# Kernel tuning notes

Measured on AMD Instinct MI355X. Metric: run time of the kernel, lower is better.

The kernel has to match this reference:

```python
import jax, jax.numpy as jnp
import numpy as np

NUM_HEADS = 8
NUM_LEVELS = 4
NUM_POINTS = 16
NUM_BEV = 2
EMBED = 256
BS = 64
NQ = NUM_LEVELS * NUM_POINTS  # 64


def _bilinear_sample(img, grid):
    """F.grid_sample(mode='bilinear', padding_mode='zeros', align_corners=False).
    img: (N, C, H, W); grid: (N, Hg, Wg, 2) in [-1, 1] (x, y). Returns (N, C, Hg, Wg)."""
    N, C, H, W = img.shape
    gx = (grid[..., 0] + 1.0) * (W * 0.5) - 0.5  # (N, Hg, Wg)
    gy = (grid[..., 1] + 1.0) * (H * 0.5) - 0.5
    x0 = jnp.floor(gx)
    y0 = jnp.floor(gy)
    flat = img.reshape(N, C, H * W)

    def gather(xi, yi):
        valid = (xi >= 0) & (xi <= W - 1) & (yi >= 0) & (yi <= H - 1)
        xc = jnp.clip(xi, 0, W - 1).astype(jnp.int32)
        yc = jnp.clip(yi, 0, H - 1).astype(jnp.int32)
        idx = (yc * W + xc).reshape(N, 1, -1)
        g = jnp.take_along_axis(flat, idx, axis=2).reshape(N, C, xi.shape[1], xi.shape[2])
        return g * valid[:, None, :, :].astype(img.dtype)

    wx1 = (gx - x0)[:, None]  # (N,1,Hg,Wg)
    wy1 = (gy - y0)[:, None]
    v00 = gather(x0, y0)
    v01 = gather(x0 + 1.0, y0)
    v10 = gather(x0, y0 + 1.0)
    v11 = gather(x0 + 1.0, y0 + 1.0)
    top = v00 * (1.0 - wx1) + v01 * wx1
    bot = v10 * (1.0 - wx1) + v11 * wx1
    return top * (1.0 - wy1) + bot * wy1


def _forward(query, key_hist, value_hist, reference_points, W_off, b_off, spatial_shapes):
    bs, nq, d = query.shape
    Hn, L, P, BEV = NUM_HEADS, NUM_LEVELS, NUM_POINTS, NUM_BEV
    dh = d // Hn
    Pb = P * BEV
    ss = np.asarray(spatial_shapes)  # (L, 2) static (h, w)

    queries = jnp.concatenate([query, query], axis=1)           # (bs, 2*nq, d)
    keies = jnp.concatenate([query, key_hist], axis=1)
    values = jnp.concatenate([query, value_hist], axis=1)
    qb = queries.shape[1]

    # sampling offsets projection (the only used learned linear in the original forward)
    off = (queries @ W_off + b_off).reshape(bs, qb, Hn, Pb, L, 2)

    # NOTE: original re-assigns q/k/v from the RAW concatenated tensors (to_Q/to_K/to_V discarded)
    qh = queries.reshape(bs, qb, Hn, dh)
    kh = keies.reshape(bs, qb, Hn, dh)
    vh = values.reshape(bs, qb, Hn, dh)

    attn = jax.nn.softmax(jnp.einsum('bqhd,bkhd->bqhk', qh, kh), axis=-1)
    attn = attn.reshape(bs, qb, Hn, L, Pb)

    rp = jnp.concatenate([reference_points, reference_points], axis=1)  # (bs, qb, L, 2)
    norm = jnp.stack([jnp.asarray(ss[:, 1], jnp.float32),
                      jnp.asarray(ss[:, 0], jnp.float32)], axis=-1)      # (L, 2) = (w, h)
    loc = rp[:, :, None, None, :, :] + off / norm                        # (bs,qb,H,Pb,L,2)
    # FAITHFUL: original uses .view here (pure reshape, not a transpose)
    loc = loc.reshape(bs, qb, Hn, L, Pb, 2)
    grids = 2.0 * loc - 1.0

    sampled = []
    start = 0
    for l in range(L):
        h_, w_ = int(ss[l, 0]), int(ss[l, 1])
        vl = vh[:, start:start + h_ * w_]                                # (bs, hw, H, dh)
        start += h_ * w_
        img = vl.transpose(0, 2, 3, 1).reshape(bs * Hn, dh, h_, w_)      # (bs*H, dh, h, w)
        grid_l = grids[:, :, :, l].transpose(0, 2, 1, 3, 4).reshape(bs * Hn, qb, Pb, 2)
        sampled.append(_bilinear_sample(img, grid_l))                    # (bs*H, dh, qb, Pb)

    samp = jnp.stack(sampled, axis=-2).reshape(bs * Hn, dh, qb, L * Pb)
    aw = attn.transpose(0, 2, 1, 3, 4).reshape(bs * Hn, 1, qb, L * Pb)
    out = (samp * aw).sum(-1)                                            # (bs*H, dh, qb)
    # FAITHFUL: original reshapes q_bev dim as (nq, BEV) and means over BEV
    out = out.reshape(bs, Hn * dh, nq, BEV).mean(-1).transpose(0, 2, 1)  # (bs, nq, d)
    return out + query  # dropout is identity at eval


def setup_inputs() -> dict:
    key = jax.random.key(0)
    ks = jax.random.split(key, 6)
    query = jax.random.normal(ks[0], (BS, NQ, EMBED), jnp.float32)
    key_hist = jax.random.normal(ks[1], (BS, NQ, EMBED), jnp.float32)
    value_hist = jax.random.normal(ks[2], (BS, NQ, EMBED), jnp.float32)
    reference_points = jax.random.uniform(ks[3], (BS, NQ, NUM_LEVELS, 2), jnp.float32)
    spatial_shapes = jnp.array([[4, 8]] * NUM_LEVELS, dtype=jnp.int32)  # sum(h*w)=128=L*P*BEV
    off_dim = NUM_HEADS * NUM_BEV * NUM_POINTS * NUM_LEVELS * 2
    W_off = jax.random.normal(ks[4], (EMBED, off_dim), jnp.float32) * 0.02
    b_off = jnp.zeros((off_dim,), jnp.float32)
    return {"query": query, "key_hist": key_hist, "value_hist": value_hist,
            "reference_points": reference_points, "spatial_shapes": spatial_shapes,
            "W_off": W_off, "b_off": b_off}


def reference(query, key_hist, value_hist, reference_points, spatial_shapes, W_off, b_off):
    return _forward(query, key_hist, value_hist, reference_points, W_off, b_off, spatial_shapes)
```

## Files before the change

### kernel.cpp

```cpp
#include <hip/hip_runtime.h>


typedef short  s16x8 __attribute__((ext_vector_type(8)));
typedef short  s16x4 __attribute__((ext_vector_type(4)));
typedef float  f32x4 __attribute__((ext_vector_type(4)));

__device__ __forceinline__ unsigned short f2bf(float f) {
    union { float f; unsigned u; } v; v.f = f;
    unsigned r = v.u + 0x7FFFu + ((v.u >> 16) & 1u);
    return (unsigned short)(r >> 16);
}
__device__ __forceinline__ float bf2f(unsigned short u) {
    return __uint_as_float(((unsigned)u) << 16);
}

__global__ __launch_bounds__(256) void prep(
    const float* __restrict__ W, const float* __restrict__ query,
    const float* __restrict__ key_hist,
    short* __restrict__ Wtb, short* __restrict__ Qb, short* __restrict__ Khb)
{
    __shared__ float s[32][33];
    const int bx = blockIdx.x, t = threadIdx.x;
    if (bx < 512) {
        const int n0 = (bx & 63) * 32, k0 = (bx >> 6) * 32;
        const int c = t & 31, r0 = t >> 5;
        #pragma unroll
        for (int p = 0; p < 4; ++p) {
            const int r = r0 + p * 8;
            s[r][c] = W[(size_t)(k0 + r) * 2048 + n0 + c];
        }
        __syncthreads();
        #pragma unroll
        for (int p = 0; p < 4; ++p) {
            const int r = r0 + p * 8;
            Wtb[(size_t)(n0 + r) * 256 + k0 + c] = (short)f2bf(s[c][r]);
        }
    } else {
        const int j = bx - 512;
        const bool isK = j >= 1024;
        const float* src = isK ? key_hist : query;
        short* dst = isK ? Khb : Qb;
        const int i4 = ((j & 1023) * 256 + t) * 4;
        const float4 v = *(const float4*)(src + i4);
        s16x4 o;
        o.x = (short)f2bf(v.x); o.y = (short)f2bf(v.y);
        o.z = (short)f2bf(v.z); o.w = (short)f2bf(v.w);
        *(s16x4*)(dst + i4) = o;
    }
}

__global__ __launch_bounds__(256, 2) void mega2(
    const float* __restrict__ query, const float* __restrict__ value_hist,
    const float* __restrict__ refp,
    const short* __restrict__ Qb, const short* __restrict__ Khb,
    const short* __restrict__ Wtb, const float* __restrict__ bias,
    float* __restrict__ out)
{
    const int h = blockIdx.x, b = blockIdx.y;
    const int t = threadIdx.x, lane = t & 63, wave = t >> 6;
    const int quad = lane >> 4, col = lane & 15;
    const int wq = wave * 16;

    __shared__ __align__(16) short VTl[32 * 136];
    __shared__ __align__(16) short attLb[64 * 136];
    __shared__ __align__(16) float rpsL[512];
    __shared__ __align__(16) float AmU[9216];
    short* Bsl = (short*)AmU;
    float* Am  = AmU;
    short* Amb = (short*)AmU;

    {
        const int p = t >> 1, hf = (t & 1) * 16;
        const float* src = ((p < 64) ? query : value_hist) +
                           (size_t)(b * 64 + (p & 63)) * 256 + h * 32 + hf;
        #pragma unroll
        for (int u = 0; u < 4; ++u) {
            const float4 v = *(const float4*)(src + 4 * u);
            VTl[(hf + 4 * u + 0) * 136 + p] = (short)f2bf(v.x);
            VTl[(hf + 4 * u + 1) * 136 + p] = (short)f2bf(v.y);
            VTl[(hf + 4 * u + 2) * 136 + p] = (short)f2bf(v.z);
            VTl[(hf + 4 * u + 3) * 136 + p] = (short)f2bf(v.w);
        }
    }
    rpsL[t]       = refp[(size_t)b * 512 + t];
    rpsL[t + 256] = refp[(size_t)b * 512 + t + 256];

    {
        const s16x8 aq = *(const s16x8*)(Qb +
            ((size_t)b * 64 + wq + col) * 256 + h * 32 + quad * 8);
        f32x4 lacc[8];
        #pragma unroll
        for (int t8 = 0; t8 < 8; ++t8) {
            const short* src = (t8 < 4)
                ? (Qb  + ((size_t)b * 64 + 16 * t8 + col) * 256)
                : (Khb + ((size_t)b * 64 + 16 * (t8 - 4) + col) * 256);
            const s16x8 bk = *(const s16x8*)(src + h * 32 + quad * 8);
            const f32x4 z = {0.f, 0.f, 0.f, 0.f};
            lacc[t8] = __builtin_amdgcn_mfma_f32_16x16x32_bf16(aq, bk, z, 0, 0, 0);
        }
        #pragma unroll
        for (int r = 0; r < 4; ++r) {
            float m = lacc[0][r];
            #pragma unroll
            for (int t8 = 1; t8 < 8; ++t8) m = fmaxf(m, lacc[t8][r]);
            #pragma unroll
            for (int s = 1; s < 16; s <<= 1) m = fmaxf(m, __shfl_xor(m, s, 64));
            float e[8], ssum = 0.f;
            #pragma unroll
            for (int t8 = 0; t8 < 8; ++t8) {
                e[t8] = __expf(lacc[t8][r] - m); ssum += e[t8];
            }
            #pragma unroll
            for (int s = 1; s < 16; s <<= 1) ssum += __shfl_xor(ssum, s, 64);
            const float inv = 1.0f / ssum;
            const int q = wq + 4 * quad + r;
            #pragma unroll
            for (int t8 = 0; t8 < 8; ++t8)
                attLb[q * 136 + 16 * t8 + col] = (short)f2bf(e[t8] * inv);
        }
    }

    f32x4 acc[4][4] = {};
    for (int kq = 0; kq < 4; ++kq) {
        s16x8 afp[4][2];
        #pragma unroll
        for (int mi = 0; mi < 4; ++mi)
            #pragma unroll
            for (int ks = 0; ks < 2; ++ks)
                afp[mi][ks] = *(const s16x8*)(Qb +
                    ((size_t)b * 64 + 16 * mi + col) * 256
                    + kq * 64 + ks * 32 + quad * 8);
        #pragma unroll
        for (int u = 0; u < 8; ++u) {
            const int g = t + 256 * u;
            const int w = g >> 9, rowu = (g >> 3) & 63, koff = (g & 7) * 8;
            *(s16x8*)&Bsl[(w * 64 + rowu) * 72 + koff] =
                *(const s16x8*)(Wtb + (size_t)(h * 256 + w * 64 + rowu) * 256
                                + kq * 64 + koff);
        }
        __syncthreads();
        #pragma unroll
        for (int ks = 0; ks < 2; ++ks) {
            s16x8 bf[4];
            #pragma unroll
            for (int nj = 0; nj < 4; ++nj)
                bf[nj] = *(const s16x8*)&Bsl[(wave * 64 + 16 * nj + col) * 72
                                             + ks * 32 + quad * 8];
            #pragma unroll
            for (int mi = 0; mi < 4; ++mi)
                #pragma unroll
                for (int nj = 0; nj < 4; ++nj)
                    acc[mi][nj] = __builtin_amdgcn_mfma_f32_16x16x32_bf16(
                        afp[mi][ks], bf[nj], acc[mi][nj], 0, 0, 0);
        }
        __syncthreads();
    }

    {
        #pragma unroll
        for (int u = 0; u < 33; ++u) AmU[t + 256 * u] = 0.f;
    }
    __syncthreads();
    {
        const int i   = col >> 1;
        const int par = col & 1;
        const int base = 32 * wave;
        #pragma unroll
        for (int nj = 0; nj < 4; ++nj) {
            const float bj = bias[h * 256 + wave * 64 + 16 * nj + col];
            const int f = 32 * wave + 8 * nj + i;
            #pragma unroll
            for (int mi = 0; mi < 4; ++mi) {
                float v[4], p[4];
                #pragma unroll
                for (int r = 0; r < 4; ++r) v[r] = acc[mi][nj][r] + bj;
                #pragma unroll
                for (int r = 0; r < 4; ++r) p[r] = __shfl_xor(v[r], 1, 64);
                #pragma unroll
                for (int rs = 0; rs < 2; ++rs) {
                    const int r = par * 2 + rs;
                    const float ox = par ? p[r] : v[r];
                    const float oy = par ? v[r] : p[r];
                    const int q = 16 * mi + 4 * quad + r;
                    const float2 rp = *(const float2*)&rpsL[q * 8 + (i & 3) * 2];
                    const float a = bf2f((unsigned short)attLb[q * 136 + f]);
                    const float gx = 8.f * (rp.x + ox * 0.125f) - 0.5f;
                    const float gy = 4.f * (rp.y + oy * 0.25f) - 0.5f;
                    const float x0f = floorf(gx), y0f = floorf(gy);
                    const float wx = gx - x0f, wy = gy - y0f;
                    const int x0 = (int)x0f, y0 = (int)y0f;
                    float* rowW = &Am[q * 132 + base];
                    const bool xv0 = (x0 >= 0) && (x0 < 8);
                    const bool xv1 = (x0 >= -1) && (x0 < 7);
                    const bool yv0 = (y0 >= 0) && (y0 < 4);
                    const bool yv1 = (y0 >= -1) && (y0 < 3);
                    if (xv0 && yv0) unsafeAtomicAdd(&rowW[y0 * 8 + x0],           a * (1.f - wx) * (1.f - wy));
                    if (xv1 && yv0) unsafeAtomicAdd(&rowW[y0 * 8 + x0 + 1],       a * wx * (1.f - wy));
                    if (xv0 && yv1) unsafeAtomicAdd(&rowW[(y0 + 1) * 8 + x0],     a * (1.f - wx) * wy);
                    if (xv1 && yv1) unsafeAtomicAdd(&rowW[(y0 + 1) * 8 + x0 + 1], a * wx * wy);
                }
            }
        }
    }
    __syncthreads();

    {
        const int cq = t >> 2, cc = (t & 3) * 32;
        float vreg[32];
        #pragma unroll
        for (int u = 0; u < 8; ++u) {
            const float4 v = *(const float4*)&Am[cq * 132 + cc + 4 * u];
            vreg[4 * u + 0] = v.x; vreg[4 * u + 1] = v.y;
            vreg[4 * u + 2] = v.z; vreg[4 * u + 3] = v.w;
        }
        __syncthreads();
        #pragma unroll
        for (int u = 0; u < 4; ++u) {
            s16x8 o;
            #pragma unroll
            for (int j = 0; j < 8; ++j) o[j] = (short)f2bf(vreg[u * 8 + j]);
            *(s16x8*)&Amb[cq * 136 + cc + u * 8] = o;
        }
    }
    __syncthreads();
    {
        f32x4 oacc[2] = {};
        #pragma unroll
        for (int ks = 0; ks < 4; ++ks) {
            const s16x8 af = *(const s16x8*)&Amb[(wq + col) * 136 + ks * 32 + quad * 8];
            #pragma unroll
            for (int n2 = 0; n2 < 2; ++n2) {
                const s16x8 bv = *(const s16x8*)&VTl[(n2 * 16 + col) * 136
                                                     + ks * 32 + quad * 8];
                oacc[n2] = __builtin_amdgcn_mfma_f32_16x16x32_bf16(af, bv, oacc[n2], 0, 0, 0);
            }
        }
        #pragma unroll
        for (int n2 = 0; n2 < 2; ++n2) {
            const int d = h * 32 + n2 * 16 + col;
            #pragma unroll
            for (int pr = 0; pr < 2; ++pr) {
                const float avg = 0.5f * (oacc[n2][2 * pr] + oacc[n2][2 * pr + 1]);
                const int pj = wave * 8 + quad * 2 + pr;
                const size_t re = ((size_t)b * 64 + pj) * 256 + d;
                const size_t ro = ((size_t)b * 64 + pj + 32) * 256 + d;
                out[re] = query[re] + avg;
                out[ro] = query[ro] + avg;
            }
        }
    }
}

extern "C" void kernel_launch(void* const* d_in, const int* in_sizes, int n_in,
                              void* d_out, int out_size, void* d_ws, size_t ws_size,
                              hipStream_t stream) {
    (void)in_sizes; (void)n_in; (void)out_size; (void)ws_size;
    const float* query      = (const float*)d_in[0];
    const float* key_hist   = (const float*)d_in[1];
    const float* value_hist = (const float*)d_in[2];
    const float* refp       = (const float*)d_in[3];
    const float* W_off      = (const float*)d_in[5];
    const float* b_off      = (const float*)d_in[6];

    char* ws = (char*)d_ws;
    short* Wtb = (short*)(ws);
    short* Qb  = (short*)(ws + (1u << 20));
    short* Khb = (short*)(ws + (3u << 20));
    float* out = (float*)d_out;

    prep<<<2560, 256, 0, stream>>>(W_off, query, key_hist, Wtb, Qb, Khb);
    mega2<<<dim3(8, 64), 256, 0, stream>>>(query, value_hist, refp,
                                           Qb, Khb, Wtb, b_off, out);
}
```

Before: 162.2 us.

## Fuse bf16 conversion prep kernel into main kernel, read fp32 inputs directly

Removes the separate prep kernel that transposed W to bf16 and converted query/key_hist to bf16 in workspace. The main kernel now loads fp32 query, key_hist and W directly from global memory and packs them to bf16 in registers before the MFMAs. It drops the LDS staging of W and its barriers, saving a launch and a workspace round trip. In exchange, W is read as strided scalar fp32 loads (8 rows at stride 2048) and converted redundantly by each of the 64 batch blocks.

```diff
diff --git a/kernel.cpp b/kernel.cpp
--- a/kernel.cpp
+++ b/kernel.cpp
@@ -2,7 +2,6 @@
 
 
 typedef short  s16x8 __attribute__((ext_vector_type(8)));
-typedef short  s16x4 __attribute__((ext_vector_type(4)));
 typedef float  f32x4 __attribute__((ext_vector_type(4)));
 
 __device__ __forceinline__ unsigned short f2bf(float f) {
@@ -13,47 +12,19 @@
 __device__ __forceinline__ float bf2f(unsigned short u) {
     return __uint_as_float(((unsigned)u) << 16);
 }
-
-__global__ __launch_bounds__(256) void prep(
-    const float* __restrict__ W, const float* __restrict__ query,
-    const float* __restrict__ key_hist,
-    short* __restrict__ Wtb, short* __restrict__ Qb, short* __restrict__ Khb)
-{
-    __shared__ float s[32][33];
-    const int bx = blockIdx.x, t = threadIdx.x;
-    if (bx < 512) {
-        const int n0 = (bx & 63) * 32, k0 = (bx >> 6) * 32;
-        const int c = t & 31, r0 = t >> 5;
-        #pragma unroll
-        for (int p = 0; p < 4; ++p) {
-            const int r = r0 + p * 8;
-            s[r][c] = W[(size_t)(k0 + r) * 2048 + n0 + c];
-        }
-        __syncthreads();
-        #pragma unroll
-        for (int p = 0; p < 4; ++p) {
-            const int r = r0 + p * 8;
-            Wtb[(size_t)(n0 + r) * 256 + k0 + c] = (short)f2bf(s[c][r]);
-        }
-    } else {
-        const int j = bx - 512;
-        const bool isK = j >= 1024;
-        const float* src = isK ? key_hist : query;
-        short* dst = isK ? Khb : Qb;
-        const int i4 = ((j & 1023) * 256 + t) * 4;
-        const float4 v = *(const float4*)(src + i4);
-        s16x4 o;
-        o.x = (short)f2bf(v.x); o.y = (short)f2bf(v.y);
-        o.z = (short)f2bf(v.z); o.w = (short)f2bf(v.w);
-        *(s16x4*)(dst + i4) = o;
-    }
-}
-
-__global__ __launch_bounds__(256, 2) void mega2(
-    const float* __restrict__ query, const float* __restrict__ value_hist,
-    const float* __restrict__ refp,
-    const short* __restrict__ Qb, const short* __restrict__ Khb,
-    const short* __restrict__ Wtb, const float* __restrict__ bias,
+__device__ __forceinline__ s16x8 pack8(const float4 a, const float4 b) {
+    s16x8 o;
+    o[0] = (short)f2bf(a.x); o[1] = (short)f2bf(a.y);
+    o[2] = (short)f2bf(a.z); o[3] = (short)f2bf(a.w);
+    o[4] = (short)f2bf(b.x); o[5] = (short)f2bf(b.y);
+    o[6] = (short)f2bf(b.z); o[7] = (short)f2bf(b.w);
+    return o;
+}
+
+__global__ __launch_bounds__(256, 2) void mega3(
+    const float* __restrict__ query, const float* __restrict__ key_hist,
+    const float* __restrict__ value_hist, const float* __restrict__ refp,
+    const float* __restrict__ W, const float* __restrict__ bias,
     float* __restrict__ out)
 {
     const int h = blockIdx.x, b = blockIdx.y;
@@ -64,11 +35,14 @@
     __shared__ __align__(16) short VTl[32 * 136];
     __shared__ __align__(16) short attLb[64 * 136];
     __shared__ __align__(16) float rpsL[512];
-    __shared__ __align__(16) float AmU[9216];
-    short* Bsl = (short*)AmU;
+    __shared__ __align__(16) float AmU[8448];
     float* Am  = AmU;
     short* Amb = (short*)AmU;
 
+    {
+        #pragma unroll
+        for (int u = 0; u < 33; ++u) AmU[t + 256 * u] = 0.f;
+    }
     {
         const int p = t >> 1, hf = (t & 1) * 16;
         const float* src = ((p < 64) ? query : value_hist) +
@@ -86,15 +60,16 @@
     rpsL[t + 256] = refp[(size_t)b * 512 + t + 256];
 
     {
-        const s16x8 aq = *(const s16x8*)(Qb +
-            ((size_t)b * 64 + wq + col) * 256 + h * 32 + quad * 8);
+        const float* qp = query + ((size_t)b * 64 + wq + col) * 256 + h * 32 + quad * 8;
+        const s16x8 aq = pack8(*(const float4*)qp, *(const float4*)(qp + 4));
         f32x4 lacc[8];
         #pragma unroll
         for (int t8 = 0; t8 < 8; ++t8) {
-            const short* src = (t8 < 4)
-                ? (Qb  + ((size_t)b * 64 + 16 * t8 + col) * 256)
-                : (Khb + ((size_t)b * 64 + 16 * (t8 - 4) + col) * 256);
-            const s16x8 bk = *(const s16x8*)(src + h * 32 + quad * 8);
+            const float* kp = ((t8 < 4)
+                ? (query    + ((size_t)b * 64 + 16 * t8 + col) * 256)
+                : (key_hist + ((size_t)b * 64 + 16 * (t8 - 4) + col) * 256))
+                + h * 32 + quad * 8;
+            const s16x8 bk = pack8(*(const float4*)kp, *(const float4*)(kp + 4));
             const f32x4 z = {0.f, 0.f, 0.f, 0.f};
             lacc[t8] = __builtin_amdgcn_mfma_f32_16x16x32_bf16(aq, bk, z, 0, 0, 0);
         }
@@ -121,46 +96,36 @@
     }
 
     f32x4 acc[4][4] = {};
-    for (int kq = 0; kq < 4; ++kq) {
-        s16x8 afp[4][2];
-        #pragma unroll
-        for (int mi = 0; mi < 4; ++mi)
-            #pragma unroll
-            for (int ks = 0; ks < 2; ++ks)
-                afp[mi][ks] = *(const s16x8*)(Qb +
-                    ((size_t)b * 64 + 16 * mi + col) * 256
-                    + kq * 64 + ks * 32 + quad * 8);
-        #pragma unroll
-        for (int u = 0; u < 8; ++u) {
-            const int g = t + 256 * u;
-            const int w = g >> 9, rowu = (g >> 3) & 63, koff = (g & 7) * 8;
-            *(s16x8*)&Bsl[(w * 64 + rowu) * 72 + koff] =
-                *(const s16x8*)(Wtb + (size_t)(h * 256 + w * 64 + rowu) * 256
-                                + kq * 64 + koff);
-        }
-        __syncthreads();
-        #pragma unroll
-        for (int ks = 0; ks < 2; ++ks) {
-            s16x8 bf[4];
-            #pragma unroll
-            for (int nj = 0; nj < 4; ++nj)
-                bf[nj] = *(const s16x8*)&Bsl[(wave * 64 + 16 * nj + col) * 72
-                                             + ks * 32 + quad * 8];
-            #pragma unroll
-            for (int mi = 0; mi < 4; ++mi)
-                #pragma unroll
-                for (int nj = 0; nj < 4; ++nj)
-                    acc[mi][nj] = __builtin_amdgcn_mfma_f32_16x16x32_bf16(
-                        afp[mi][ks], bf[nj], acc[mi][nj], 0, 0, 0);
-        }
-        __syncthreads();
-    }
-
-    {
-        #pragma unroll
-        for (int u = 0; u < 33; ++u) AmU[t + 256 * u] = 0.f;
+    {
+        const int nbase = h * 256 + wave * 64;
+        #pragma unroll
+        for (int kq = 0; kq < 4; ++kq) {
+            #pragma unroll
+            for (int ks = 0; ks < 2; ++ks) {
+                const int k0 = kq * 64 + ks * 32 + quad * 8;
+                s16x8 af[4];
+                #pragma unroll
+                for (int mi = 0; mi < 4; ++mi) {
+                    const float* ap = query + ((size_t)b * 64 + 16 * mi + col) * 256 + k0;
+                    af[mi] = pack8(*(const float4*)ap, *(const float4*)(ap + 4));
+                }
+                #pragma unroll
+                for (int nj = 0; nj < 4; ++nj) {
+                    const float* wp = W + (size_t)k0 * 2048 + nbase + 16 * nj + col;
+                    s16x8 bfv;
+                    #pragma unroll
+                    for (int j = 0; j < 8; ++j)
+                        bfv[j] = (short)f2bf(wp[(size_t)j * 2048]);
+                    #pragma unroll
+                    for (int mi = 0; mi < 4; ++mi)
+                        acc[mi][nj] = __builtin_amdgcn_mfma_f32_16x16x32_bf16(
+                            af[mi], bfv, acc[mi][nj], 0, 0, 0);
+                }
+            }
+        }
     }
     __syncthreads();
+
     {
         const int i   = col >> 1;
         const int par = col & 1;
@@ -254,21 +219,15 @@
 extern "C" void kernel_launch(void* const* d_in, const int* in_sizes, int n_in,
                               void* d_out, int out_size, void* d_ws, size_t ws_size,
                               hipStream_t stream) {
-    (void)in_sizes; (void)n_in; (void)out_size; (void)ws_size;
+    (void)in_sizes; (void)n_in; (void)out_size; (void)d_ws; (void)ws_size;
     const float* query      = (const float*)d_in[0];
     const float* key_hist   = (const float*)d_in[1];
     const float* value_hist = (const float*)d_in[2];
     const float* refp       = (const float*)d_in[3];
     const float* W_off      = (const float*)d_in[5];
     const float* b_off      = (const float*)d_in[6];
-
-    char* ws = (char*)d_ws;
-    short* Wtb = (short*)(ws);
-    short* Qb  = (short*)(ws + (1u << 20));
-    short* Khb = (short*)(ws + (3u << 20));
     float* out = (float*)d_out;
 
-    prep<<<2560, 256, 0, stream>>>(W_off, query, key_hist, Wtb, Qb, Khb);
-    mega2<<<dim3(8, 64), 256, 0, stream>>>(query, value_hist, refp,
-                                           Qb, Khb, Wtb, b_off, out);
-}
+    mega3<<<dim3(8, 64), 256, 0, stream>>>(query, key_hist, value_hist,
+                                           refp, W_off, b_off, out);
+}
```

Result: slower. 165.7 us (+2.2%).
